# Performance work log

Measured on AMD Instinct MI355X. Metric: run time of the kernel, lower is better.

The kernel has to match this reference:

```python
import jax, jax.numpy as jnp
import numpy as np

# LeNet-5 custom connectivity between S2 (6 ch) and C3 (16 ch): MAP[i, o] = 1 if input ch i feeds output ch o
MAP_INFO = np.array([
    [1, 0, 0, 0, 1, 1, 1, 0, 0, 1, 1, 1, 1, 0, 1, 1],
    [1, 1, 0, 0, 0, 1, 1, 1, 0, 0, 1, 1, 1, 1, 0, 1],
    [1, 1, 1, 0, 0, 0, 1, 1, 1, 0, 0, 1, 0, 1, 1, 1],
    [0, 1, 1, 1, 0, 0, 1, 1, 1, 1, 0, 0, 1, 0, 1, 1],
    [0, 0, 1, 1, 1, 0, 0, 1, 1, 1, 1, 0, 1, 1, 0, 1],
    [0, 0, 0, 1, 1, 1, 0, 0, 1, 1, 1, 1, 0, 1, 1, 1],
], dtype=np.float32)  # [6, 16]

SCALE = 1.7159
SLOPE = 2.0 / 3.0


def _conv(x, w):
    # x: [B, Cin, H, W], w: [Cout, Cin, kh, kw], VALID padding, stride 1
    return jax.lax.conv_general_dilated(
        x, w, window_strides=(1, 1), padding='VALID',
        dimension_numbers=('NCHW', 'OIHW', 'NCHW'))


def _subsample(x, w, b):
    # 2x2 average pool then per-channel affine (trainable scale/bias)
    B, C, H, W = x.shape
    p = x.reshape(B, C, H // 2, 2, W // 2, 2).mean(axis=(3, 5))
    return p * w[None, :, None, None] + b[None, :, None, None]


def _act(x):
    return SCALE * jnp.tanh(SLOPE * x)


def setup_inputs() -> dict:
    key = jax.random.key(0)
    ks = jax.random.split(key, 16)
    B = 8192

    def unif(k, shape, fan_in):
        return (jax.random.uniform(k, shape, dtype=jnp.float32) * 4.8 - 2.4) / fan_in

    x = jax.random.normal(ks[0], (B, 1, 32, 32), dtype=jnp.float32)
    c1_w = unif(ks[1], (6, 1, 5, 5), 25 * 1)
    c1_b = jax.random.uniform(ks[2], (6,), dtype=jnp.float32) * 0.1
    s2_w = unif(ks[3], (6,), 4)
    s2_b = jax.random.uniform(ks[4], (6,), dtype=jnp.float32)
    c3_w = unif(ks[5], (16, 6, 5, 5), 25 * 6)
    c3_b = jax.random.uniform(ks[6], (16,), dtype=jnp.float32) * 0.1
    s4_w = unif(ks[7], (16,), 4)
    s4_b = jax.random.uniform(ks[8], (16,), dtype=jnp.float32)
    c5_w = unif(ks[9], (120, 16, 5, 5), 25 * 16)
    c5_b = jax.random.uniform(ks[10], (120,), dtype=jnp.float32) * 0.1
    f6_w = unif(ks[11], (84, 120), 120)
    f6_b = jax.random.uniform(ks[12], (84,), dtype=jnp.float32) * 0.1
    rbf_w = jax.random.uniform(ks[13], (84, 10), dtype=jnp.float32)
    return dict(x=x, c1_w=c1_w, c1_b=c1_b, s2_w=s2_w, s2_b=s2_b,
                c3_w=c3_w, c3_b=c3_b, s4_w=s4_w, s4_b=s4_b,
                c5_w=c5_w, c5_b=c5_b, f6_w=f6_w, f6_b=f6_b, rbf_w=rbf_w)


def reference(x, c1_w, c1_b, s2_w, s2_b, c3_w, c3_b, s4_w, s4_b,
              c5_w, c5_b, f6_w, f6_b, rbf_w):
    # C1: 1->6 conv5, replicate padding 2 -> [B,6,32,32]
    xp = jnp.pad(x, ((0, 0), (0, 0), (2, 2), (2, 2)), mode='edge')
    h = _conv(xp, c1_w) + c1_b[None, :, None, None]
    # S2 + squashing act -> [B,6,16,16]
    h = _act(_subsample(h, s2_w, s2_b))
    # C3: sparse-connectivity conv expressed as dense conv with masked weights -> [B,16,12,12]
    mask = jnp.asarray(MAP_INFO.T)[:, :, None, None]  # [16,6,1,1]
    h = _conv(h, c3_w * mask) + c3_b[None, :, None, None]
    # S4 + act -> [B,16,6,6]
    h = _act(_subsample(h, s4_w, s4_b))
    # C5: 16->120 conv5 -> [B,120,1,1]
    h = _conv(h, c5_w) + c5_b[None, :, None, None]
    h = h.reshape(-1, 120)
    # F6 + act -> [B,84]
    h = _act(h @ f6_w.T + f6_b)
    # RBF output: squared euclidean distance to class prototypes -> [B,10]
    out = jnp.sum((h[:, :, None] - rbf_w[None, :, :]) ** 2, axis=1)
    return out
```

## Files before the change

### kernel.cpp

```cpp
#include <hip/hip_runtime.h>
#include <math.h>

typedef _Float16 h16;
typedef h16  h8v __attribute__((ext_vector_type(8)));
typedef h16  h4v __attribute__((ext_vector_type(4)));
typedef h16  h2v __attribute__((ext_vector_type(2)));
typedef float f4v __attribute__((ext_vector_type(4)));

#if defined(__has_builtin)
#if __has_builtin(__builtin_amdgcn_fdot2)
#define FDOT2(a,b,c) __builtin_amdgcn_fdot2((a),(b),(c),false)
#endif
#endif
#ifndef FDOT2
#define FDOT2(a,b,c) ((c) + (float)(a).x*(float)(b).x + (float)(a).y*(float)(b).y)
#endif

#define WS_K1H  0
#define WS_B1   216
#define WS_B3   224
#define WS_W3H  240
#define WS_W5H  2544
#define WS_F6H  35312

#define L_RBF   0
#define L_B3    3360
#define L_C5B   3424
#define L_F6B   3936
#define L_S2H   4352
#define L_A6    4352
#define L_HB    8704
#define L_XPADH 18176
#define L_AI    18176
#define L_A5    18176
#define L_S4    34816
#define LDS_TOTAL 39936

__device__ const unsigned char MASK16[16] = {7,14,28,56,49,35,15,30,60,57,51,39,27,54,45,63};

__device__ __forceinline__ float squash(float x) {
    float z = (2.0f / 3.0f) * x;
    float a = fabsf(z);
    float e = __expf(-2.0f * a);
    float t = (1.0f - e) * __builtin_amdgcn_rcpf(1.0f + e);
    return copysignf(1.7159f * t, z);
}

__global__ __launch_bounds__(256) void prep_kernel(
    const float* __restrict__ c1_w, const float* __restrict__ c1_b,
    const float* __restrict__ s2_w, const float* __restrict__ s2_b,
    const float* __restrict__ c3_w, const float* __restrict__ c3_b,
    const float* __restrict__ s4_w, const float* __restrict__ s4_b,
    const float* __restrict__ c5_w, const float* __restrict__ f6_w,
    float* __restrict__ ws)
{
    const int gid = blockIdx.x * 256 + threadIdx.x;
    const int gstr = gridDim.x * 256;
    h16* K1H = (h16*)ws;
    for (int idx = gid; idx < 216; idx += gstr) {
        int c = idx / 36, r = idx - c * 36;
        int u = r / 6, v = r - u * 6;
        float s = 0.f;
        #pragma unroll
        for (int dy = 0; dy < 2; ++dy)
            #pragma unroll
            for (int dx = 0; dx < 2; ++dx) {
                int ky = u - dy, kx = v - dx;
                if (ky >= 0 && ky < 5 && kx >= 0 && kx < 5)
                    s += c1_w[(c * 5 + ky) * 5 + kx];
            }
        K1H[idx] = (h16)(0.25f * s * s2_w[c]);
    }
    if (gid < 6)  ws[WS_B1 + gid] = s2_w[gid] * c1_b[gid] + s2_b[gid];
    if (gid < 16) ws[WS_B3 + gid] = s4_w[gid] * c3_b[gid] + s4_b[gid];
    h16* W3H = (h16*)(ws + WS_W3H);
    for (int idx = gid; idx < 4608; idx += gstr) {
        int i = idx / 768, r = idx - i * 768;
        int n = r / 48, k = r - n * 48;
        float val = 0.f;
        if (k < 36) {
            int u = k / 6, v = k - u * 6;
            float s = 0.f;
            #pragma unroll
            for (int dy = 0; dy < 2; ++dy)
                #pragma unroll
                for (int dx = 0; dx < 2; ++dx) {
                    int ky = u - dy, kx = v - dx;
                    if (ky >= 0 && ky < 5 && kx >= 0 && kx < 5)
                        s += c3_w[((n * 6 + i) * 5 + ky) * 5 + kx];
                }
            val = ((MASK16[n] >> i) & 1) ? 0.25f * s4_w[n] * s : 0.f;
        }
        W3H[idx] = (h16)val;
    }
    h16* W5H = (h16*)(ws + WS_W5H);
    for (int idx = gid; idx < 65536; idx += gstr) {
        int i = idx >> 12, r = idx & 4095;
        int n = r >> 5, k = r & 31;
        float val = (n < 120 && k < 25) ? c5_w[n * 400 + i * 25 + k] : 0.f;
        W5H[idx] = (h16)val;
    }
    h16* F6H = (h16*)(ws + WS_F6H);
    for (int idx = gid; idx < 12288; idx += gstr) {
        int n = idx >> 7, k = idx & 127;
        float val = (n < 84 && k < 120) ? f6_w[n * 120 + k] : 0.f;
        F6H[idx] = (h16)val;
    }
}

__global__ __launch_bounds__(256, 4) void lenet_kernel(
    const float* __restrict__ x,
    const float* __restrict__ c5_b, const float* __restrict__ f6_b,
    const float* __restrict__ rbf_w,
    const float* __restrict__ ws,
    float* __restrict__ out)
{
    __shared__ __align__(16) char smem[LDS_TOTAL];
    float* s_rbf = (float*)(smem + L_RBF);
    float* s_b3  = (float*)(smem + L_B3);
    float* s_c5b = (float*)(smem + L_C5B);
    float* s_f6b = (float*)(smem + L_F6B);
    h16*  XPADH  = (h16*)(smem + L_XPADH);
    h16*  S2H    = (h16*)(smem + L_S2H);
    h16*  AI     = (h16*)(smem + L_AI);
    h16*  S4     = (h16*)(smem + L_S4);
    h16*  A5     = (h16*)(smem + L_A5);
    h16*  A6     = (h16*)(smem + L_A6);
    float* HB    = (float*)(smem + L_HB);

    const int tid  = threadIdx.x;
    const int wave = __builtin_amdgcn_readfirstlane(tid >> 6);
    const int lane = tid & 63;
    const int quad = lane >> 4;
    const int lr   = lane & 15;

    for (int idx = tid; idx < 840; idx += 256) {
        int k = idx / 10, c = idx - k * 10;
        s_rbf[c * 84 + k] = rbf_w[idx];
    }
    if (tid < 16)  s_b3[tid] = ws[WS_B3 + tid];
    if (tid < 128) s_c5b[tid] = (tid < 120) ? c5_b[tid] : 0.f;
    if (tid < 96)  s_f6b[tid] = (tid < 84) ? f6_b[tid] : 0.f;
    const float* xb = x + (size_t)blockIdx.x * 4096;
    for (int idx = tid; idx < 2880; idx += 256) {
        int img = idx / 720, r2 = idx - img * 720;
        int u = r2 / 20, v2 = r2 - u * 20;
        int sy = min(max(u - 2, 0), 31);
        int c0 = min(max(2 * v2 - 2, 0), 31);
        int c1 = min(max(2 * v2 - 1, 0), 31);
        const float* xr = xb + img * 1024 + sy * 32;
        h2v hv; hv.x = (h16)xr[c0]; hv.y = (h16)xr[c1];
        *(h2v*)(XPADH + img * 1440 + u * 40 + 2 * v2) = hv;
    }
    __syncthreads();

    {
        int py = tid >> 4, px = tid & 15;
        h2v win2[4][18];
        #pragma unroll
        for (int img = 0; img < 4; ++img) {
            const h16* basep = XPADH + img * 1440 + (2 * py) * 40 + 2 * px;
            #pragma unroll
            for (int u = 0; u < 6; ++u)
                #pragma unroll
                for (int p = 0; p < 3; ++p)
                    win2[img][u * 3 + p] = *(const h2v*)(basep + u * 40 + 2 * p);
        }
        const h2v* K1H = (const h2v*)ws;
        #pragma unroll
        for (int c = 0; c < 6; ++c) {
            float bias = ws[WS_B1 + c];
            h2v wv[18];
            #pragma unroll
            for (int j = 0; j < 18; ++j) wv[j] = K1H[c * 18 + j];
            #pragma unroll
            for (int img = 0; img < 4; ++img) {
                float acc = bias;
                #pragma unroll
                for (int j = 0; j < 18; ++j)
                    acc = FDOT2(win2[img][j], wv[j], acc);
                S2H[img * 1728 + c * 288 + py * 18 + px] = (h16)squash(acc);
            }
        }
    }
    __syncthreads();

    {
        const h16* W3H = (const h16*)(ws + WS_W3H);
        h8v w3a[6]; h4v w3b[6];
        #pragma unroll
        for (int i = 0; i < 6; ++i) {
            const h16* bbase = W3H + i * 768 + lr * 48;
            w3a[i] = *(const h8v*)(bbase + quad * 8);
            w3b[i] = *(const h4v*)(bbase + 32 + quad * 4);
        }
        for (int t = tid; t < 1440; t += 256) {
            int row = t / 10, j = t - row * 10;
            *(unsigned int*)(AI + row * 56 + 36 + 2 * j) = 0u;
        }
        const int rowv = (tid < 144) ? tid : 0;
        const int imgR = rowv / 36, posR = rowv - imgR * 36;
        const int pyR = posR / 6, pxR = posR - pyR * 6;
        const h16* srcR = S2H + imgR * 1728 + (2 * pyR) * 18 + 2 * pxR;
        h16* dstR = AI + rowv * 56;
        f4v cacc[3] = {};
        for (int i = 0; i < 6; ++i) {
            if (tid < 144) {
                const h16* src = srcR + i * 288;
                #pragma unroll
                for (int u = 0; u < 6; ++u) {
                    *(unsigned int*)(dstR + u * 6)     = *(const unsigned int*)(src + u * 18);
                    *(unsigned int*)(dstR + u * 6 + 2) = *(const unsigned int*)(src + u * 18 + 2);
                    *(unsigned int*)(dstR + u * 6 + 4) = *(const unsigned int*)(src + u * 18 + 4);
                }
            }
            __syncthreads();
            #pragma unroll
            for (int s = 0; s < 3; ++s) {
                int Mt = wave + 4 * s;
                if (Mt < 9) {
                    const h16* ar = AI + (Mt * 16 + lr) * 56;
                    h8v a8 = *(const h8v*)(ar + quad * 8);
                    cacc[s] = __builtin_amdgcn_mfma_f32_16x16x32_f16(a8, w3a[i], cacc[s], 0, 0, 0);
                    h4v a4 = *(const h4v*)(ar + 32 + quad * 4);
                    cacc[s] = __builtin_amdgcn_mfma_f32_16x16x16f16(a4, w3b[i], cacc[s], 0, 0, 0);
                }
            }
            if (i < 5) __syncthreads();
        }
        #pragma unroll
        for (int s = 0; s < 3; ++s) {
            int Mt = wave + 4 * s;
            if (Mt < 9) {
                #pragma unroll
                for (int r = 0; r < 4; ++r) {
                    int m = Mt * 16 + quad * 4 + r;
                    int img = m / 36, pos = m - img * 36;
                    float v = cacc[s][r] + s_b3[lr];
                    S4[img * 640 + lr * 40 + pos] = (h16)squash(v);
                }
            }
        }
    }
    __syncthreads();

    {
        for (int t = tid; t < 8192; t += 256) {
            int k = t & 31, i = (t >> 5) & 15, m = t >> 9;
            h16 v = (h16)0.f;
            if (k < 25) {
                int r = k / 5, c = k - r * 5;
                int img = m >> 2, q = m & 3, qy = q >> 1, qx = q & 1;
                v = S4[img * 640 + i * 40 + (qy + r) * 6 + qx + c];
            }
            A5[m * 520 + i * 32 + k] = v;
        }
        __syncthreads();
        const h16* W5H = (const h16*)(ws + WS_W5H);
        f4v dacc[2] = {};
        #pragma unroll 4
        for (int i = 0; i < 16; ++i) {
            h8v bf0 = *(const h8v*)(W5H + i * 4096 + (wave * 32 + lr) * 32 + quad * 8);
            h8v bf1 = *(const h8v*)(W5H + i * 4096 + (wave * 32 + 16 + lr) * 32 + quad * 8);
            h8v af0 = *(const h8v*)(A5 + lr * 520 + i * 32 + quad * 8);
            dacc[0] = __builtin_amdgcn_mfma_f32_16x16x32_f16(af0, bf0, dacc[0], 0, 0, 0);
            dacc[1] = __builtin_amdgcn_mfma_f32_16x16x32_f16(af0, bf1, dacc[1], 0, 0, 0);
        }
        if (tid < 128) {
            int m = tid >> 3, c = 120 + (tid & 7);
            A6[m * 136 + c] = (h16)0.f;
        }
        #pragma unroll
        for (int nt = 0; nt < 2; ++nt) {
            int n = wave * 32 + nt * 16 + lr;
            if (n < 120) {
                int tt = n / 30, cb = (n - tt * 30) * 4;
                float bias = s_c5b[n];
                #pragma unroll
                for (int r = 0; r < 4; ++r) {
                    int m = quad * 4 + r;
                    int img = m >> 2, q = m & 3;
                    A6[(img * 4 + tt) * 136 + cb + q] = (h16)(dacc[nt][r] + bias);
                }
            }
        }
    }
    __syncthreads();

    {
        const h16* F6H = (const h16*)(ws + WS_F6H);
        f4v eacc[2] = {};
        #pragma unroll
        for (int kc = 0; kc < 4; ++kc) {
            h8v a8 = *(const h8v*)(A6 + lr * 136 + kc * 32 + quad * 8);
            h8v b0 = *(const h8v*)(F6H + (wave * 16 + lr) * 128 + kc * 32 + quad * 8);
            eacc[0] = __builtin_amdgcn_mfma_f32_16x16x32_f16(a8, b0, eacc[0], 0, 0, 0);
            if (wave < 2) {
                h8v b1 = *(const h8v*)(F6H + ((wave + 4) * 16 + lr) * 128 + kc * 32 + quad * 8);
                eacc[1] = __builtin_amdgcn_mfma_f32_16x16x32_f16(a8, b1, eacc[1], 0, 0, 0);
            }
        }
        {
            int n = wave * 16 + lr;
            float bias = s_f6b[n];
            #pragma unroll
            for (int r = 0; r < 4; ++r) {
                int m = quad * 4 + r;
                HB[m * 88 + n] = squash(eacc[0][r] + bias);
            }
        }
        if (wave < 2) {
            int n = (wave + 4) * 16 + lr;
            if (n < 84) {
                float bias = s_f6b[n];
                #pragma unroll
                for (int r = 0; r < 4; ++r) {
                    int m = quad * 4 + r;
                    HB[m * 88 + n] = squash(eacc[1][r] + bias);
                }
            }
        }
    }
    __syncthreads();

    if (tid < 160) {
        int m = tid / 10, cls = tid - m * 10;
        const float4* hr = (const float4*)(HB + m * 88);
        const float4* pr = (const float4*)(s_rbf + cls * 84);
        float a = 0.f;
        #pragma unroll
        for (int u = 0; u < 21; ++u) {
            float4 hv = hr[u], pv = pr[u];
            float dx = hv.x - pv.x, dy = hv.y - pv.y;
            float dz = hv.z - pv.z, dw = hv.w - pv.w;
            a += dx * dx + dy * dy + dz * dz + dw * dw;
        }
        out[(size_t)blockIdx.x * 160 + tid] = a;
    }
}

extern "C" void kernel_launch(void* const* d_in, const int* in_sizes, int n_in,
                              void* d_out, int out_size, void* d_ws, size_t ws_size,
                              hipStream_t stream) {
    (void)n_in; (void)out_size; (void)ws_size;
    const float* x     = (const float*)d_in[0];
    const float* c1_w  = (const float*)d_in[1];
    const float* c1_b  = (const float*)d_in[2];
    const float* s2_w  = (const float*)d_in[3];
    const float* s2_b  = (const float*)d_in[4];
    const float* c3_w  = (const float*)d_in[5];
    const float* c3_b  = (const float*)d_in[6];
    const float* s4_w  = (const float*)d_in[7];
    const float* s4_b  = (const float*)d_in[8];
    const float* c5_w  = (const float*)d_in[9];
    const float* c5_b  = (const float*)d_in[10];
    const float* f6_w  = (const float*)d_in[11];
    const float* f6_b  = (const float*)d_in[12];
    const float* rbf_w = (const float*)d_in[13];
    float* out = (float*)d_out;
    float* ws  = (float*)d_ws;

    const int B = in_sizes[0] / 1024;

    prep_kernel<<<256, 256, 0, stream>>>(c1_w, c1_b, s2_w, s2_b, c3_w, c3_b,
                                         s4_w, s4_b, c5_w, f6_w, ws);
    lenet_kernel<<<B / 4, 256, 0, stream>>>(x, c5_b, f6_b, rbf_w, ws, out);
}
```

Baseline: 160.5 us.

## Shrink LDS footprint, move RBF prototypes to workspace, vectorize LDS staging

The per-block transposed RBF prototype copy in shared memory is replaced by a transposed copy written once to the workspace by the prep kernel and read from global memory. The shared-memory layout is repacked so S2H, S4 and HB alias each other, which cuts the LDS footprint, and launch bounds are raised from 4 to 5 blocks per SM to allow more resident blocks. The C3 im2col copy, the C5 im2col gather and the A6 padding zero-fill are rewritten to use wider vector LDS stores, with the S4 stride padded. The risks are register pressure under the tighter launch bound and global loads in the RBF stage.

```diff
diff --git a/kernel.cpp b/kernel.cpp
--- a/kernel.cpp
+++ b/kernel.cpp
@@ -6,6 +6,9 @@
 typedef h16  h4v __attribute__((ext_vector_type(4)));
 typedef h16  h2v __attribute__((ext_vector_type(2)));
 typedef float f4v __attribute__((ext_vector_type(4)));
+typedef unsigned int u32;
+typedef u32  u4v __attribute__((ext_vector_type(4)));
+typedef u32  u2v __attribute__((ext_vector_type(2)));
 
 #if defined(__has_builtin)
 #if __has_builtin(__builtin_amdgcn_fdot2)
@@ -22,19 +25,19 @@
 #define WS_W3H  240
 #define WS_W5H  2544
 #define WS_F6H  35312
-
-#define L_RBF   0
-#define L_B3    3360
-#define L_C5B   3424
-#define L_F6B   3936
-#define L_S2H   4352
-#define L_A6    4352
-#define L_HB    8704
-#define L_XPADH 18176
-#define L_AI    18176
-#define L_A5    18176
-#define L_S4    34816
-#define LDS_TOTAL 39936
+#define WS_RBFT 41456
+
+#define L_B3    0
+#define L_C5B   64
+#define L_F6B   576
+#define L_S2H   960
+#define L_S4    960
+#define L_HB    960
+#define L_A6    6592
+#define L_XPADH 14784
+#define L_AI    14784
+#define L_A5    14784
+#define LDS_TOTAL 31424
 
 __device__ const unsigned char MASK16[16] = {7,14,28,56,49,35,15,30,60,57,51,39,27,54,45,63};
 
@@ -52,6 +55,7 @@
     const float* __restrict__ c3_w, const float* __restrict__ c3_b,
     const float* __restrict__ s4_w, const float* __restrict__ s4_b,
     const float* __restrict__ c5_w, const float* __restrict__ f6_w,
+    const float* __restrict__ rbf_w,
     float* __restrict__ ws)
 {
     const int gid = blockIdx.x * 256 + threadIdx.x;
@@ -106,17 +110,19 @@
         float val = (n < 84 && k < 120) ? f6_w[n * 120 + k] : 0.f;
         F6H[idx] = (h16)val;
     }
+    for (int idx = gid; idx < 840; idx += gstr) {
+        int k = idx / 10, c = idx - k * 10;
+        ws[WS_RBFT + c * 84 + k] = rbf_w[idx];
+    }
 }
 
-__global__ __launch_bounds__(256, 4) void lenet_kernel(
+__global__ __launch_bounds__(256, 5) void lenet_kernel(
     const float* __restrict__ x,
     const float* __restrict__ c5_b, const float* __restrict__ f6_b,
-    const float* __restrict__ rbf_w,
     const float* __restrict__ ws,
     float* __restrict__ out)
 {
     __shared__ __align__(16) char smem[LDS_TOTAL];
-    float* s_rbf = (float*)(smem + L_RBF);
     float* s_b3  = (float*)(smem + L_B3);
     float* s_c5b = (float*)(smem + L_C5B);
     float* s_f6b = (float*)(smem + L_F6B);
@@ -134,10 +140,6 @@
     const int quad = lane >> 4;
     const int lr   = lane & 15;
 
-    for (int idx = tid; idx < 840; idx += 256) {
-        int k = idx / 10, c = idx - k * 10;
-        s_rbf[c * 84 + k] = rbf_w[idx];
-    }
     if (tid < 16)  s_b3[tid] = ws[WS_B3 + tid];
     if (tid < 128) s_c5b[tid] = (tid < 120) ? c5_b[tid] : 0.f;
     if (tid < 96)  s_f6b[tid] = (tid < 84) ? f6_b[tid] : 0.f;
@@ -196,7 +198,7 @@
         }
         for (int t = tid; t < 1440; t += 256) {
             int row = t / 10, j = t - row * 10;
-            *(unsigned int*)(AI + row * 56 + 36 + 2 * j) = 0u;
+            *(u32*)(AI + row * 56 + 36 + 2 * j) = 0u;
         }
         const int rowv = (tid < 144) ? tid : 0;
         const int imgR = rowv / 36, posR = rowv - imgR * 36;
@@ -207,12 +209,18 @@
         for (int i = 0; i < 6; ++i) {
             if (tid < 144) {
                 const h16* src = srcR + i * 288;
+                u32 wrow[18];
                 #pragma unroll
                 for (int u = 0; u < 6; ++u) {
-                    *(unsigned int*)(dstR + u * 6)     = *(const unsigned int*)(src + u * 18);
-                    *(unsigned int*)(dstR + u * 6 + 2) = *(const unsigned int*)(src + u * 18 + 2);
-                    *(unsigned int*)(dstR + u * 6 + 4) = *(const unsigned int*)(src + u * 18 + 4);
-                }
+                    wrow[u*3+0] = *(const u32*)(src + u * 18);
+                    wrow[u*3+1] = *(const u32*)(src + u * 18 + 2);
+                    wrow[u*3+2] = *(const u32*)(src + u * 18 + 4);
+                }
+                *(u4v*)(dstR)      = (u4v){wrow[0],  wrow[1],  wrow[2],  wrow[3]};
+                *(u4v*)(dstR + 8)  = (u4v){wrow[4],  wrow[5],  wrow[6],  wrow[7]};
+                *(u4v*)(dstR + 16) = (u4v){wrow[8],  wrow[9],  wrow[10], wrow[11]};
+                *(u4v*)(dstR + 24) = (u4v){wrow[12], wrow[13], wrow[14], wrow[15]};
+                *(u2v*)(dstR + 32) = (u2v){wrow[16], wrow[17]};
             }
             __syncthreads();
             #pragma unroll
@@ -237,7 +245,7 @@
                     int m = Mt * 16 + quad * 4 + r;
                     int img = m / 36, pos = m - img * 36;
                     float v = cacc[s][r] + s_b3[lr];
-                    S4[img * 640 + lr * 40 + pos] = (h16)squash(v);
+                    S4[img * 672 + lr * 42 + pos] = (h16)squash(v);
                 }
             }
         }
@@ -245,15 +253,21 @@
     __syncthreads();
 
     {
-        for (int t = tid; t < 8192; t += 256) {
-            int k = t & 31, i = (t >> 5) & 15, m = t >> 9;
-            h16 v = (h16)0.f;
-            if (k < 25) {
-                int r = k / 5, c = k - r * 5;
-                int img = m >> 2, q = m & 3, qy = q >> 1, qx = q & 1;
-                v = S4[img * 640 + i * 40 + (qy + r) * 6 + qx + c];
-            }
-            A5[m * 520 + i * 32 + k] = v;
+        {
+            int m = tid >> 4, i = tid & 15;
+            int img = m >> 2, q = m & 3, qy = q >> 1, qx = q & 1;
+            const h16* s4b = S4 + img * 672 + i * 42 + qy * 6 + qx;
+            h16* dst = A5 + m * 520 + i * 32;
+            #pragma unroll
+            for (int c = 0; c < 4; ++c) {
+                h8v v;
+                #pragma unroll
+                for (int j = 0; j < 8; ++j) {
+                    int k = c * 8 + j;
+                    v[j] = (k < 25) ? s4b[(k / 5) * 6 + (k % 5)] : (h16)0.f;
+                }
+                *(h8v*)(dst + c * 8) = v;
+            }
         }
         __syncthreads();
         const h16* W5H = (const h16*)(ws + WS_W5H);
@@ -266,9 +280,9 @@
             dacc[0] = __builtin_amdgcn_mfma_f32_16x16x32_f16(af0, bf0, dacc[0], 0, 0, 0);
             dacc[1] = __builtin_amdgcn_mfma_f32_16x16x32_f16(af0, bf1, dacc[1], 0, 0, 0);
         }
-        if (tid < 128) {
-            int m = tid >> 3, c = 120 + (tid & 7);
-            A6[m * 136 + c] = (h16)0.f;
+        if (tid < 64) {
+            int m = tid >> 2, j = tid & 3;
+            *(u32*)(A6 + m * 136 + 120 + 2 * j) = 0u;
         }
         #pragma unroll
         for (int nt = 0; nt < 2; ++nt) {
@@ -326,7 +340,7 @@
     if (tid < 160) {
         int m = tid / 10, cls = tid - m * 10;
         const float4* hr = (const float4*)(HB + m * 88);
-        const float4* pr = (const float4*)(s_rbf + cls * 84);
+        const float4* pr = (const float4*)(ws + WS_RBFT + cls * 84);
         float a = 0.f;
         #pragma unroll
         for (int u = 0; u < 21; ++u) {
@@ -363,6 +377,6 @@
     const int B = in_sizes[0] / 1024;
 
     prep_kernel<<<256, 256, 0, stream>>>(c1_w, c1_b, s2_w, s2_b, c3_w, c3_b,
-                                         s4_w, s4_b, c5_w, f6_w, ws);
-    lenet_kernel<<<B / 4, 256, 0, stream>>>(x, c5_b, f6_b, rbf_w, ws, out);
+                                         s4_w, s4_b, c5_w, f6_w, rbf_w, ws);
+    lenet_kernel<<<B / 4, 256, 0, stream>>>(x, c5_b, f6_b, ws, out);
 }
```

After: 149.4 us. -6.9%, faster.
